# Optimization experiments

Measured on AMD Instinct MI355X. Metric: run time of the kernel, lower is better.

## Reference

```python
import math
import jax, jax.numpy as jnp
import numpy as np

NH, D, MULT, VOCAB, NLAYER = 4, 256, 128, 256, 2
N = MULT * D // NH  # 8192
EPS = 1e-5
THETA = 2.0 ** 16


def get_freqs(n):
    q = (jnp.arange(n, dtype=jnp.float32) // 2) * 2  # quantize(t, 2)
    return 1.0 / (THETA ** (q / n)) / (2 * math.pi)


def ln(x):
    # LayerNorm over last dim, no affine
    mu = jnp.mean(x, axis=-1, keepdims=True)
    var = jnp.mean((x - mu) ** 2, axis=-1, keepdims=True)
    return (x - mu) / jnp.sqrt(var + EPS)


def rope(phases, v):
    # phases: (T, N), v: (B, nh, T, N)
    ph = (phases % 1.0) * (2 * math.pi)
    c, s = jnp.cos(ph), jnp.sin(ph)
    v_rot = jnp.stack((-v[..., 1::2], v[..., ::2]), axis=-1).reshape(v.shape)
    return v * c + v_rot * s


def setup_inputs() -> dict:
    key = jax.random.key(0)
    ks = jax.random.split(key, 6)
    std = 0.02
    return {
        "idx": jax.random.randint(ks[0], (1, 2048), 0, VOCAB),
        "embed": jax.random.normal(ks[1], (VOCAB, D), jnp.float32) * std,
        "encoder": jax.random.normal(ks[2], (NH, D, N), jnp.float32) * std,
        "encoder_v": jax.random.normal(ks[3], (NH, D, N), jnp.float32) * std,
        "decoder": jax.random.normal(ks[4], (NH * N, D), jnp.float32) * std,
        "lm_head": jax.random.normal(ks[5], (D, VOCAB), jnp.float32) * std,
    }


def reference(idx, embed, encoder, encoder_v, decoder, lm_head):
    B, T = idx.shape
    freqs = get_freqs(N)  # (N,)
    phases = jnp.arange(T, dtype=jnp.float32)[:, None] * freqs[None, :]  # (T, N)
    # strictly-lower-triangular causal mask (tril diagonal=-1)
    t = jnp.arange(T)
    mask = (t[:, None] > t[None, :]).astype(jnp.float32)  # (T, T)

    x = ln(embed[idx][:, None])  # (B, 1, T, D)
    for _ in range(NLAYER):
        x_sparse = jax.nn.relu(jnp.einsum('bltd,hdn->bhtn', x, encoder))  # (B,nh,T,N)
        QR = rope(phases, x_sparse)
        scores = jnp.einsum('bhtn,bhsn->bhts', QR, QR) * mask  # (B,nh,T,T)
        yKV = ln(jnp.einsum('bhts,blsd->bhtd', scores, x))  # (B,nh,T,D)
        y_sparse = jax.nn.relu(jnp.einsum('bhtd,hdn->bhtn', yKV, encoder_v))
        xy = x_sparse * y_sparse  # (B,nh,T,N)
        xy = xy.transpose(0, 2, 1, 3).reshape(B, 1, T, NH * N)
        yMLP = xy @ decoder  # (B,1,T,D)
        x = ln(x + ln(yMLP))
    logits = x[:, 0] @ lm_head  # (B,T,vocab)
    return logits
```

## Files before the change

kernel.cpp:

```cpp
#include <hip/hip_runtime.h>
#include <hip/hip_bf16.h>
#include <math.h>

typedef unsigned short u16;
typedef unsigned int u32;
typedef __attribute__((ext_vector_type(8))) short short8;
typedef __attribute__((ext_vector_type(4))) float f32x4;

__device__ __forceinline__ u16 f2b(float f) {
  u32 u = __builtin_bit_cast(u32, f);
  u = (u + 0x7fffu + ((u >> 16) & 1u)) >> 16;
  return (u16)u;
}
__device__ __forceinline__ float b2f(u16 s) {
  return __builtin_bit_cast(float, (u32)s << 16);
}

__device__ __forceinline__ void ld_g2l(const u16* g, u16* l) {
  __builtin_amdgcn_global_load_lds(
      (const __attribute__((address_space(1))) unsigned int*)g,
      (__attribute__((address_space(3))) unsigned int*)l, 16, 0, 0);
}

__device__ __forceinline__ void gemm_core(
    const u16* __restrict__ A, const u16* __restrict__ B,
    int lda, int ldb, int Klen, int kb, int bm, int bn,
    u16* __restrict__ As, u16* __restrict__ Bs, f32x4 (&acc)[4][4])
{
  int tid = threadIdx.x;
  int w = tid >> 6, lane = tid & 63;
  int srow = (w << 4) + (lane >> 2);
  int scol = (lane & 3) << 3;
  const u16* ga0 = A + (long)(bm * 128 + srow) * lda + kb + scol;
  const u16* ga1 = ga0 + (long)64 * lda;
  const u16* gb0 = B + (long)(bn * 128 + srow) * ldb + kb + scol;
  const u16* gb1 = gb0 + (long)64 * ldb;
  u16* la0 = As + (w << 9);  u16* la1 = la0 + 2048;
  u16* lb0 = Bs + (w << 9);  u16* lb1 = lb0 + 2048;

  int wm = (w >> 1) << 6, wn = (w & 1) << 6;
  int lane15 = lane & 15, quad = lane >> 4;
  const u16* ar = As + (wm + lane15) * 32 + quad * 8;
  const u16* br = Bs + (wn + lane15) * 32 + quad * 8;

#pragma unroll
  for (int i = 0; i < 4; i++)
#pragma unroll
    for (int j = 0; j < 4; j++) { f32x4 z = {0.f, 0.f, 0.f, 0.f}; acc[i][j] = z; }

  for (int k = 0; k < Klen; k += 32) {
    ld_g2l(ga0 + k, la0);
    ld_g2l(ga1 + k, la1);
    ld_g2l(gb0 + k, lb0);
    ld_g2l(gb1 + k, lb1);
    __syncthreads();
    short8 af[4], bfr[4];
#pragma unroll
    for (int mt = 0; mt < 4; mt++) af[mt] = *(const short8*)(ar + mt * 16 * 32);
#pragma unroll
    for (int nt = 0; nt < 4; nt++) bfr[nt] = *(const short8*)(br + nt * 16 * 32);
#pragma unroll
    for (int mt = 0; mt < 4; mt++)
#pragma unroll
      for (int nt = 0; nt < 4; nt++)
        acc[mt][nt] = __builtin_amdgcn_mfma_f32_16x16x32_bf16(af[mt], bfr[nt], acc[mt][nt], 0, 0, 0);
    __syncthreads();
  }
}

__device__ __forceinline__ void rope_cs(int n, int t, float& c, float& s) {
  float f = exp2f((float)(-(n & ~1)) * (1.0f / 512.0f)) * 0.15915494f;
  float ph = (float)t * f;
  ph -= floorf(ph);
  __sincosf(ph * 6.2831853f, &s, &c);
}

template<int EPI>
__global__ __launch_bounds__(256, 2) void gemm_bt(
    const u16* __restrict__ A, const u16* __restrict__ B, void* __restrict__ C,
    int K, int lda, int ldb, int ldc, int nsplits, long aB, long bB, long cB,
    int tri)
{
  __shared__ __align__(16) u16 As[128 * 32];
  __shared__ __align__(16) u16 Bs[128 * 32];
  int bn = blockIdx.x, bm = blockIdx.y;
  int batch = blockIdx.z / nsplits, sp = blockIdx.z % nsplits;
  int Klen = K / nsplits, kb = sp * Klen;
  if (tri) {
    int kend = (bm + 1) * 128;
    if (kb >= kend) return;
    if (kb + Klen > kend) Klen = kend - kb;
  }

  f32x4 acc[4][4];
  gemm_core(A + (long)batch * aB, B + (long)batch * bB, lda, ldb, Klen, kb, bm, bn, As, Bs, acc);

  int lane = threadIdx.x & 63, w = threadIdx.x >> 6;
  int wm = (w >> 1) << 6, wn = (w & 1) << 6;
  int lane15 = lane & 15, quad = lane >> 4;

#pragma unroll
  for (int mt = 0; mt < 4; mt++)
#pragma unroll
    for (int nt = 0; nt < 4; nt++) {
      int gn = bn * 128 + wn + nt * 16 + lane15;
#pragma unroll
      for (int r = 0; r < 4; r++) {
        int gm = bm * 128 + wm + mt * 16 + quad * 4 + r;
        float v = acc[mt][nt][r];
        long ci = (long)batch * cB + (long)gm * ldc + gn;
        if (EPI == 0) {
          ((float*)C)[ci] = v;
        } else if (EPI == 1) {
          float rv = fmaxf(v, 0.f);
          float ro = __shfl_xor(rv, 1);
          float c, s; rope_cs(gn, gm, c, s);
          float out = (gn & 1) ? (rv * c + ro * s) : (rv * c - ro * s);
          ((u16*)C)[ci] = f2b(out);
        } else if (EPI == 3) {
          atomicAdd(&((float*)C)[ci], v);
        } else if (EPI == 4) {
          u16* Cp = (u16*)C;
          float q = b2f(Cp[ci]);
          float qo = __shfl_xor(q, 1);
          float c, s; rope_cs(gn, gm, c, s);
          float xs = (gn & 1) ? (q * c - qo * s) : (q * c + qo * s);
          Cp[ci] = f2b(fmaxf(v, 0.f) * xs);
        }
      }
    }
}

__global__ __launch_bounds__(512, 2) void gemm_scores(
    const u16* __restrict__ QR, u16* __restrict__ S, int T)
{
  __shared__ __align__(16) u16 lds[4][128 * 32];
  int bn = blockIdx.x, bm = blockIdx.y;
  u16* Sb = S + (long)blockIdx.z * (long)T * T;
  int tid = threadIdx.x;

  if (bn > bm) {
    for (int i = tid; i < 128 * 128 / 8; i += 512) {
      int r = i >> 4, c8 = (i & 15) << 3;
      *(uint4*)(&Sb[(long)(bm * 128 + r) * T + bn * 128 + c8]) = make_uint4(0u, 0u, 0u, 0u);
    }
    return;
  }

  const u16* Q = QR + (long)blockIdx.z * (long)T * 8192;
  int w = tid >> 6, lane = tid & 63;
  int srow = (w << 4) + (lane >> 2);
  int scol = (lane & 3) << 3;
  const u16* ga = Q + (long)(bm * 128 + srow) * 8192 + scol;
  const u16* gb = Q + (long)(bn * 128 + srow) * 8192 + scol;
  u16* lA0 = lds[0] + (w << 9);
  u16* lA1 = lds[1] + (w << 9);
  u16* lB0 = lds[2] + (w << 9);
  u16* lB1 = lds[3] + (w << 9);

  int q = w & 3, half = w >> 2;
  int wm = (q >> 1) << 6, wn = (q & 1) << 6;
  int lane15 = lane & 15, quad = lane >> 4;
  const u16* ar = lds[half] + (wm + lane15) * 32 + quad * 8;
  const u16* br = lds[2 + half] + (wn + lane15) * 32 + quad * 8;

  f32x4 acc[4][4];
#pragma unroll
  for (int i = 0; i < 4; i++)
#pragma unroll
    for (int j = 0; j < 4; j++) { f32x4 z = {0.f, 0.f, 0.f, 0.f}; acc[i][j] = z; }

  for (int k = 0; k < 8192; k += 64) {
    ld_g2l(ga + k, lA0);
    ld_g2l(ga + k + 32, lA1);
    ld_g2l(gb + k, lB0);
    ld_g2l(gb + k + 32, lB1);
    __syncthreads();
    short8 af[4], bfr[4];
#pragma unroll
    for (int mt = 0; mt < 4; mt++) af[mt] = *(const short8*)(ar + mt * 16 * 32);
#pragma unroll
    for (int nt = 0; nt < 4; nt++) bfr[nt] = *(const short8*)(br + nt * 16 * 32);
#pragma unroll
    for (int mt = 0; mt < 4; mt++)
#pragma unroll
      for (int nt = 0; nt < 4; nt++)
        acc[mt][nt] = __builtin_amdgcn_mfma_f32_16x16x32_bf16(af[mt], bfr[nt], acc[mt][nt], 0, 0, 0);
    __syncthreads();
  }

  float* red = (float*)&lds[0][0];
#pragma unroll
  for (int round = 0; round < 2; round++) {
    if (half == 1 && (q >> 1) == round) {
      float* dst = red + ((q & 1) * 64 + lane) * 64;
#pragma unroll
      for (int i = 0; i < 4; i++)
#pragma unroll
        for (int j = 0; j < 4; j++) *(f32x4*)(dst + (i * 4 + j) * 4) = acc[i][j];
    }
    __syncthreads();
    if (half == 0 && (q >> 1) == round) {
      float* src = red + ((q & 1) * 64 + lane) * 64;
#pragma unroll
      for (int i = 0; i < 4; i++)
#pragma unroll
        for (int j = 0; j < 4; j++) {
          f32x4 t = *(f32x4*)(src + (i * 4 + j) * 4);
          acc[i][j] += t;
        }
    }
    __syncthreads();
  }

  if (half == 0) {
#pragma unroll
    for (int mt = 0; mt < 4; mt++)
#pragma unroll
      for (int nt = 0; nt < 4; nt++)
#pragma unroll
        for (int r = 0; r < 4; r++) {
          int gm = bm * 128 + wm + mt * 16 + quad * 4 + r;
          int gn = bn * 128 + wn + nt * 16 + lane15;
          Sb[(long)gm * T + gn] = f2b(gm > gn ? acc[mt][nt][r] : 0.f);
        }
  }
}

__global__ __launch_bounds__(256) void trans_f32_bf16(
    const float* __restrict__ src, u16* __restrict__ dst, int R, int C)
{
  __shared__ float tile[32][33];
  long off = (long)blockIdx.z * R * C;
  const float* s = src + off;
  u16* d = dst + off;
  int lx = threadIdx.x & 31, ly = threadIdx.x >> 5;
  int c = blockIdx.x * 32 + lx;
#pragma unroll
  for (int p = 0; p < 32; p += 8)
    tile[ly + p][lx] = s[(long)(blockIdx.y * 32 + ly + p) * C + c];
  __syncthreads();
  int rr = blockIdx.y * 32 + lx;
#pragma unroll
  for (int p = 0; p < 32; p += 8)
    d[(long)(blockIdx.x * 32 + ly + p) * R + rr] = f2b(tile[lx][ly + p]);
}

__device__ __forceinline__ float block_sum(float v, float* red) {
#pragma unroll
  for (int o = 32; o > 0; o >>= 1) v += __shfl_down(v, o, 64);
  int lane = threadIdx.x & 63, wid = threadIdx.x >> 6;
  if (lane == 0) red[wid] = v;
  __syncthreads();
  float r = red[0] + red[1] + red[2] + red[3];
  __syncthreads();
  return r;
}

__global__ __launch_bounds__(256) void embed_ln(
    const int* __restrict__ idx, const float* __restrict__ embed,
    float* __restrict__ x, u16* __restrict__ xb, u16* __restrict__ xT, int T)
{
  __shared__ float red[4];
  int t = blockIdx.x, d = threadIdx.x;
  float v = embed[(long)idx[t] * 256 + d];
  float mu = block_sum(v, red) * (1.f / 256.f);
  float c = v - mu;
  float var = block_sum(c * c, red) * (1.f / 256.f);
  float o = c * rsqrtf(var + 1e-5f);
  x[(long)t * 256 + d] = o;
  xb[(long)t * 256 + d] = f2b(o);
  xT[(long)d * T + t] = f2b(o);
}

__global__ __launch_bounds__(256) void row_ln(
    const float* __restrict__ in, u16* __restrict__ out)
{
  __shared__ float red[4];
  long row = blockIdx.x;
  int d = threadIdx.x;
  float v = in[row * 256 + d];
  float mu = block_sum(v, red) * (1.f / 256.f);
  float c = v - mu;
  float var = block_sum(c * c, red) * (1.f / 256.f);
  out[row * 256 + d] = f2b(c * rsqrtf(var + 1e-5f));
}

__global__ __launch_bounds__(256) void resid_ln(
    const float* __restrict__ yMLP, float* __restrict__ x,
    u16* __restrict__ xb, u16* __restrict__ xT, int T)
{
  __shared__ float red[4];
  int t = blockIdx.x, d = threadIdx.x;
  float y = yMLP[(long)t * 256 + d];
  float mu1 = block_sum(y, red) * (1.f / 256.f);
  float c1 = y - mu1;
  float var1 = block_sum(c1 * c1, red) * (1.f / 256.f);
  float l1 = c1 * rsqrtf(var1 + 1e-5f);
  float v = x[(long)t * 256 + d] + l1;
  float mu2 = block_sum(v, red) * (1.f / 256.f);
  float c2 = v - mu2;
  float var2 = block_sum(c2 * c2, red) * (1.f / 256.f);
  float o = c2 * rsqrtf(var2 + 1e-5f);
  x[(long)t * 256 + d] = o;
  xb[(long)t * 256 + d] = f2b(o);
  xT[(long)d * T + t] = f2b(o);
}

extern "C" void kernel_launch(void* const* d_in, const int* in_sizes, int n_in,
                              void* d_out, int out_size, void* d_ws, size_t ws_size,
                              hipStream_t stream) {
  const int*   idx       = (const int*)d_in[0];
  const float* embed     = (const float*)d_in[1];
  const float* encoder   = (const float*)d_in[2];
  const float* encoder_v = (const float*)d_in[3];
  const float* decoder   = (const float*)d_in[4];
  const float* lm_head   = (const float*)d_in[5];
  const int T = in_sizes[0];
  const int D = 256, NH = 4, Nn = 8192, V = 256;

  char* ws = (char*)d_ws;
  size_t off = 0;
  auto alloc = [&](size_t bytes) -> void* {
    void* p = ws + off; off += (bytes + 255) & ~(size_t)255; return p;
  };
  float* x_f32   = (float*)alloc((size_t)T * D * 4);
  float* yMLP    = (float*)alloc((size_t)T * D * 4);
  float* yKV_f32 = (float*)alloc((size_t)NH * T * D * 4);
  u16* x_b    = (u16*)alloc((size_t)T * D * 2);
  u16* xT     = (u16*)alloc((size_t)T * D * 2);
  u16* yKV_b  = (u16*)alloc((size_t)NH * T * D * 2);
  u16* lmT    = (u16*)alloc((size_t)D * V * 2);
  u16* encT   = (u16*)alloc((size_t)NH * Nn * D * 2);
  u16* encvT  = (u16*)alloc((size_t)NH * Nn * D * 2);
  u16* decT   = (u16*)alloc((size_t)D * NH * Nn * 2);
  size_t per_head = ((size_t)T * T * 2 + 256) + ((size_t)T * Nn * 2 + 256);
  int HB = 4;
  while (HB > 1 && off + (size_t)HB * per_head > ws_size) HB >>= 1;
  u16* scores = (u16*)alloc((size_t)HB * T * T * 2);
  u16* QRxy   = (u16*)alloc((size_t)HB * T * Nn * 2);
  if (off > ws_size) return;

  trans_f32_bf16<<<dim3(Nn / 32, D / 32, NH), 256, 0, stream>>>(encoder, encT, D, Nn);
  trans_f32_bf16<<<dim3(Nn / 32, D / 32, NH), 256, 0, stream>>>(encoder_v, encvT, D, Nn);
  trans_f32_bf16<<<dim3(D / 32, (NH * Nn) / 32, 1), 256, 0, stream>>>(decoder, decT, NH * Nn, D);
  trans_f32_bf16<<<dim3(V / 32, D / 32, 1), 256, 0, stream>>>(lm_head, lmT, D, V);

  embed_ln<<<T, 256, 0, stream>>>(idx, embed, x_f32, x_b, xT, T);

  for (int l = 0; l < 2; l++) {
    hipMemsetAsync(yMLP, 0, (size_t)T * D * 4, stream);
    for (int h0 = 0; h0 < NH; h0 += HB) {
      gemm_bt<1><<<dim3(Nn / 128, T / 128, HB), 256, 0, stream>>>(
          x_b, encT + (size_t)h0 * Nn * D, QRxy,
          D, D, D, Nn, 1, 0L, (long)Nn * D, (long)T * Nn, 0);
      gemm_scores<<<dim3(T / 128, T / 128, HB), 512, 0, stream>>>(QRxy, scores, T);
      hipMemsetAsync(yKV_f32, 0, (size_t)HB * T * D * 4, stream);
      gemm_bt<3><<<dim3(D / 128, T / 128, HB * 8), 256, 0, stream>>>(
          scores, xT, yKV_f32,
          T, T, T, D, 8, (long)T * T, 0L, (long)T * D, 1);
      row_ln<<<HB * T, 256, 0, stream>>>(yKV_f32, yKV_b);
      gemm_bt<4><<<dim3(Nn / 128, T / 128, HB), 256, 0, stream>>>(
          yKV_b, encvT + (size_t)h0 * Nn * D, QRxy,
          D, D, D, Nn, 1, (long)T * D, (long)Nn * D, (long)T * Nn, 0);
      gemm_bt<3><<<dim3(D / 128, T / 128, HB * 8), 256, 0, stream>>>(
          QRxy, decT + (size_t)h0 * Nn, yMLP,
          Nn, Nn, NH * Nn, D, 8, (long)T * Nn, (long)Nn, 0L, 0);
    }
    resid_ln<<<T, 256, 0, stream>>>(yMLP, x_f32, x_b, xT, T);
  }

  gemm_bt<0><<<dim3(V / 128, T / 128, 1), 256, 0, stream>>>(
      x_b, lmT, d_out, D, D, D, V, 1, 0L, 0L, 0L, 0);
}
```

Baseline: 1.311 ms.

## Rewrite scores GEMM as 256x256 triangular-grid kernel with pipelined LDS staging

Replaces the 128x128 scores kernel, which split K across two wave halves and reduced through LDS, with a 256x256-tile kernel. Each of its 8 waves owns a 128x64 sub-tile, and the kernel double-buffers swizzled LDS tiles with interleaved global-to-LDS loads, explicit waitcnt/barrier scheduling and MFMA priority bumps. The grid is now the lower triangle only, so no blocks are spent writing zero upper tiles. This cuts redundant tile loads and reduction overhead and overlaps memory with compute. The cost is far fewer blocks (144), which can leave CUs idle, and upper-triangle tiles of the scores buffer are no longer written.

```diff
diff --git a/kernel.cpp b/kernel.cpp
--- a/kernel.cpp
+++ b/kernel.cpp
@@ -131,100 +131,132 @@
     }
 }
 
-__global__ __launch_bounds__(512, 2) void gemm_scores(
+#define SC_BAR   __builtin_amdgcn_s_barrier()
+#define SC_LGKM0 asm volatile("s_waitcnt lgkmcnt(0)" ::: "memory")
+#define SC_LGKM8 asm volatile("s_waitcnt lgkmcnt(8)" ::: "memory")
+#define SC_VMF   do { asm volatile("s_waitcnt vmcnt(4)" ::: "memory"); \
+                      __builtin_amdgcn_sched_barrier(0); } while (0)
+#define SC_P1    __builtin_amdgcn_s_setprio(1)
+#define SC_P0    __builtin_amdgcn_s_setprio(0)
+
+#define DSA(Ab, mh) { \
+  _Pragma("unroll") for (int mt = 0; mt < 4; mt++) { \
+    aA[mt][0] = *(const short8*)((Ab) + ((mh) * 64 + mt * 16) * 64 + koff0); \
+    aA[mt][1] = *(const short8*)((Ab) + ((mh) * 64 + mt * 16) * 64 + koff1); } }
+
+#define DSB(Bb, nh, dst) { \
+  _Pragma("unroll") for (int nt = 0; nt < 2; nt++) { \
+    dst[nt][0] = *(const short8*)((Bb) + ((nh) * 32 + nt * 16) * 64 + koff0); \
+    dst[nt][1] = *(const short8*)((Bb) + ((nh) * 32 + nt * 16) * 64 + koff1); } }
+
+#define MMA(MH, NH, BB) { \
+  _Pragma("unroll") for (int mt = 0; mt < 4; mt++) \
+  _Pragma("unroll") for (int nt = 0; nt < 2; nt++) { \
+    acc[(MH)*4+mt][(NH)*2+nt] = __builtin_amdgcn_mfma_f32_16x16x32_bf16( \
+        aA[mt][0], BB[nt][0], acc[(MH)*4+mt][(NH)*2+nt], 0, 0, 0); \
+    acc[(MH)*4+mt][(NH)*2+nt] = __builtin_amdgcn_mfma_f32_16x16x32_bf16( \
+        aA[mt][1], BB[nt][1], acc[(MH)*4+mt][(NH)*2+nt], 0, 0, 0); } }
+
+__global__ __launch_bounds__(512, 1) void gemm_scores8(
     const u16* __restrict__ QR, u16* __restrict__ S, int T)
 {
-  __shared__ __align__(16) u16 lds[4][128 * 32];
-  int bn = blockIdx.x, bm = blockIdx.y;
+  __shared__ __align__(16) u16 Abuf[2][256 * 64];
+  __shared__ __align__(16) u16 Bbuf[2][256 * 64];
+
+  int q = blockIdx.x;
+  int bm = (int)((sqrtf(8.f * (float)q + 1.f) - 1.f) * 0.5f);
+  while ((bm + 1) * (bm + 2) / 2 <= q) bm++;
+  while (bm * (bm + 1) / 2 > q) bm--;
+  int bn = q - bm * (bm + 1) / 2;
+
+  const u16* Q = QR + (long)blockIdx.z * (long)T * 8192;
   u16* Sb = S + (long)blockIdx.z * (long)T * T;
+
   int tid = threadIdx.x;
-
-  if (bn > bm) {
-    for (int i = tid; i < 128 * 128 / 8; i += 512) {
-      int r = i >> 4, c8 = (i & 15) << 3;
-      *(uint4*)(&Sb[(long)(bm * 128 + r) * T + bn * 128 + c8]) = make_uint4(0u, 0u, 0u, 0u);
+  int w = tid >> 6, lane = tid & 63;
+  int wr = w >> 2, wc = w & 3;
+  int lane15 = lane & 15, quad = lane >> 4;
+  int swz = lane15 & 7;
+  int koff0 = ((quad) ^ swz) << 3;
+  int koff1 = ((4 + quad) ^ swz) << 3;
+
+  const u16* gA = Q + (long)(bm * 256) * 8192;
+  const u16* gB = Q + (long)(bn * 256) * 8192;
+
+  const u16* A0 = &Abuf[0][(wr * 128 + lane15) * 64];
+  const u16* A1 = &Abuf[1][(wr * 128 + lane15) * 64];
+  const u16* B0 = &Bbuf[0][(wc * 64 + lane15) * 64];
+  const u16* B1 = &Bbuf[1][(wc * 64 + lane15) * 64];
+
+  int sr = lane >> 3, sc = lane & 7;
+  long g_sk = (long)sr * 8192 + ((sc ^ sr) << 3);
+  int l_base = (w * 16) * 64;
+  long g_wrow = (long)(w * 16) * 8192;
+
+  auto STG = [&](const u16* gHalfBase, u16* lHalfBase, int kt) {
+    const u16* g = gHalfBase + g_wrow + g_sk + kt * 64;
+    u16* l = lHalfBase + l_base;
+    ld_g2l(g, l);
+    ld_g2l(g + (long)8 * 8192, l + 8 * 64);
+  };
+
+  f32x4 acc[8][4];
+#pragma unroll
+  for (int i2 = 0; i2 < 8; i2++)
+#pragma unroll
+    for (int j = 0; j < 4; j++) { f32x4 z = {0.f, 0.f, 0.f, 0.f}; acc[i2][j] = z; }
+
+  const long HSTEP = (long)128 * 8192;
+
+  STG(gA, &Abuf[0][0], 0); STG(gA + HSTEP, &Abuf[0][128 * 64], 0);
+  STG(gB, &Bbuf[0][0], 0); STG(gB + HSTEP, &Bbuf[0][128 * 64], 0);
+  STG(gB, &Bbuf[1][0], 1); STG(gB + HSTEP, &Bbuf[1][128 * 64], 1);
+  SC_VMF;
+  SC_BAR;
+
+  const int nkt = 8192 / 64;
+  for (int i = 0; i < nkt / 2; i++) {
+    int kt1 = 2 * i + 1;
+    int kt2 = 2 * i + 2; if (kt2 > nkt - 1) kt2 = nkt - 1;
+    int kt3 = 2 * i + 3; if (kt3 > nkt - 1) kt3 = nkt - 1;
+    short8 aA[4][2], bb0[2][2], bb1[2][2];
+
+    DSA(A0, 0); DSB(B0, 0, bb0);
+    STG(gA, &Abuf[1][0], kt1);
+    SC_LGKM8; SC_BAR; SC_LGKM0; SC_P1; MMA(0, 0, bb0); SC_P0; SC_BAR;
+    DSB(B0, 1, bb1);
+    STG(gA + HSTEP, &Abuf[1][128 * 64], kt1);
+    SC_BAR; SC_LGKM0; SC_P1; MMA(0, 1, bb1); SC_P0; SC_BAR;
+    DSA(A0, 1);
+    STG(gB, &Bbuf[0][0], kt2);
+    SC_BAR; SC_LGKM0; SC_P1; MMA(1, 1, bb1); SC_P0; SC_BAR;
+    STG(gB + HSTEP, &Bbuf[0][128 * 64], kt2);
+    SC_VMF; SC_BAR; SC_LGKM0; SC_P1; MMA(1, 0, bb0); SC_P0; SC_BAR;
+
+    DSA(A1, 0); DSB(B1, 0, bb0);
+    STG(gA, &Abuf[0][0], kt2);
+    SC_LGKM8; SC_BAR; SC_LGKM0; SC_P1; MMA(0, 0, bb0); SC_P0; SC_BAR;
+    DSB(B1, 1, bb1);
+    STG(gA + HSTEP, &Abuf[0][128 * 64], kt2);
+    SC_BAR; SC_LGKM0; SC_P1; MMA(0, 1, bb1); SC_P0; SC_BAR;
+    DSA(A1, 1);
+    STG(gB, &Bbuf[1][0], kt3);
+    SC_BAR; SC_LGKM0; SC_P1; MMA(1, 1, bb1); SC_P0; SC_BAR;
+    STG(gB + HSTEP, &Bbuf[1][128 * 64], kt3);
+    SC_VMF; SC_BAR; SC_LGKM0; SC_P1; MMA(1, 0, bb0); SC_P0; SC_BAR;
+  }
+
+#pragma unroll
+  for (int mt = 0; mt < 8; mt++)
+#pragma unroll
+    for (int nt = 0; nt < 4; nt++) {
+      int gn = bn * 256 + wc * 64 + nt * 16 + lane15;
+#pragma unroll
+      for (int r = 0; r < 4; r++) {
+        int gm = bm * 256 + wr * 128 + mt * 16 + quad * 4 + r;
+        Sb[(long)gm * T + gn] = f2b(gm > gn ? acc[mt][nt][r] : 0.f);
+      }
     }
-    return;
-  }
-
-  const u16* Q = QR + (long)blockIdx.z * (long)T * 8192;
-  int w = tid >> 6, lane = tid & 63;
-  int srow = (w << 4) + (lane >> 2);
-  int scol = (lane & 3) << 3;
-  const u16* ga = Q + (long)(bm * 128 + srow) * 8192 + scol;
-  const u16* gb = Q + (long)(bn * 128 + srow) * 8192 + scol;
-  u16* lA0 = lds[0] + (w << 9);
-  u16* lA1 = lds[1] + (w << 9);
-  u16* lB0 = lds[2] + (w << 9);
-  u16* lB1 = lds[3] + (w << 9);
-
-  int q = w & 3, half = w >> 2;
-  int wm = (q >> 1) << 6, wn = (q & 1) << 6;
-  int lane15 = lane & 15, quad = lane >> 4;
-  const u16* ar = lds[half] + (wm + lane15) * 32 + quad * 8;
-  const u16* br = lds[2 + half] + (wn + lane15) * 32 + quad * 8;
-
-  f32x4 acc[4][4];
-#pragma unroll
-  for (int i = 0; i < 4; i++)
-#pragma unroll
-    for (int j = 0; j < 4; j++) { f32x4 z = {0.f, 0.f, 0.f, 0.f}; acc[i][j] = z; }
-
-  for (int k = 0; k < 8192; k += 64) {
-    ld_g2l(ga + k, lA0);
-    ld_g2l(ga + k + 32, lA1);
-    ld_g2l(gb + k, lB0);
-    ld_g2l(gb + k + 32, lB1);
-    __syncthreads();
-    short8 af[4], bfr[4];
-#pragma unroll
-    for (int mt = 0; mt < 4; mt++) af[mt] = *(const short8*)(ar + mt * 16 * 32);
-#pragma unroll
-    for (int nt = 0; nt < 4; nt++) bfr[nt] = *(const short8*)(br + nt * 16 * 32);
-#pragma unroll
-    for (int mt = 0; mt < 4; mt++)
-#pragma unroll
-      for (int nt = 0; nt < 4; nt++)
-        acc[mt][nt] = __builtin_amdgcn_mfma_f32_16x16x32_bf16(af[mt], bfr[nt], acc[mt][nt], 0, 0, 0);
-    __syncthreads();
-  }
-
-  float* red = (float*)&lds[0][0];
-#pragma unroll
-  for (int round = 0; round < 2; round++) {
-    if (half == 1 && (q >> 1) == round) {
-      float* dst = red + ((q & 1) * 64 + lane) * 64;
-#pragma unroll
-      for (int i = 0; i < 4; i++)
-#pragma unroll
-        for (int j = 0; j < 4; j++) *(f32x4*)(dst + (i * 4 + j) * 4) = acc[i][j];
-    }
-    __syncthreads();
-    if (half == 0 && (q >> 1) == round) {
-      float* src = red + ((q & 1) * 64 + lane) * 64;
-#pragma unroll
-      for (int i = 0; i < 4; i++)
-#pragma unroll
-        for (int j = 0; j < 4; j++) {
-          f32x4 t = *(f32x4*)(src + (i * 4 + j) * 4);
-          acc[i][j] += t;
-        }
-    }
-    __syncthreads();
-  }
-
-  if (half == 0) {
-#pragma unroll
-    for (int mt = 0; mt < 4; mt++)
-#pragma unroll
-      for (int nt = 0; nt < 4; nt++)
-#pragma unroll
-        for (int r = 0; r < 4; r++) {
-          int gm = bm * 128 + wm + mt * 16 + quad * 4 + r;
-          int gn = bn * 128 + wn + nt * 16 + lane15;
-          Sb[(long)gm * T + gn] = f2b(gm > gn ? acc[mt][nt][r] : 0.f);
-        }
-  }
 }
 
 __global__ __launch_bounds__(256) void trans_f32_bf16(
@@ -348,13 +380,15 @@
 
   embed_ln<<<T, 256, 0, stream>>>(idx, embed, x_f32, x_b, xT, T);
 
+  const int nbm = T / 256, ntri = nbm * (nbm + 1) / 2;
+
   for (int l = 0; l < 2; l++) {
     hipMemsetAsync(yMLP, 0, (size_t)T * D * 4, stream);
     for (int h0 = 0; h0 < NH; h0 += HB) {
       gemm_bt<1><<<dim3(Nn / 128, T / 128, HB), 256, 0, stream>>>(
           x_b, encT + (size_t)h0 * Nn * D, QRxy,
           D, D, D, Nn, 1, 0L, (long)Nn * D, (long)T * Nn, 0);
-      gemm_scores<<<dim3(T / 128, T / 128, HB), 512, 0, stream>>>(QRxy, scores, T);
+      gemm_scores8<<<dim3(ntri, 1, HB), 512, 0, stream>>>(QRxy, scores, T);
       hipMemsetAsync(yKV_f32, 0, (size_t)HB * T * D * 4, stream);
       gemm_bt<3><<<dim3(D / 128, T / 128, HB * 8), 256, 0, stream>>>(
           scores, xT, yKV_f32,
```

Measured after the change: 1.214 ms. 7.4% less time.
